# Optimization experiments

Hardware: AMD Instinct MI355X
Metric: run time of the kernel (lower is better)

Reference implementation:

```python
import math
import jax, jax.numpy as jnp
import numpy as np

SR = 48000
FRAME_HOP = 240
F0_MIN = 20.0
F0_MAX = 5000.0
F0_BINS = 64
VEL_DIM = 8
N_HARM = 128
NOISE_FFT = 1024
N_NOISE = NOISE_FFT // 2 + 1
HOP = NOISE_FFT // 4
PAD = NOISE_FFT // 2


def lin_interp(x, size):
    # matches F.interpolate(mode='linear', align_corners=False) along last axis
    T_in = x.shape[-1]
    pos = (jnp.arange(size, dtype=jnp.float32) + 0.5) * (T_in / size) - 0.5
    pos = jnp.clip(pos, 0.0, T_in - 1.0)
    lo = jnp.floor(pos).astype(jnp.int32)
    hi = jnp.minimum(lo + 1, T_in - 1)
    fr = pos - lo.astype(jnp.float32)
    return x[..., lo] * (1.0 - fr) + x[..., hi] * fr


def encode_f0(f0):
    f0s = jnp.clip(f0, F0_MIN, None)
    fn = jnp.clip((jnp.log(f0s) - math.log(F0_MIN)) / (math.log(F0_MAX) - math.log(F0_MIN)), 0.0, 1.0)
    i = jnp.arange(1, F0_BINS // 2 + 1, dtype=jnp.float32)
    ang = math.pi * i * fn[..., None]  # (B,T,bins/2)
    enc = jnp.stack([jnp.sin(ang), jnp.cos(ang)], axis=-1).reshape(f0.shape + (F0_BINS,))
    return enc * (f0 > 0).astype(jnp.float32)[..., None]


def encode_velocity(vel):
    vn = jnp.clip(vel.astype(jnp.float32) / 7.0, 0.0, 1.0)
    i = jnp.arange(1, VEL_DIM // 2 + 1, dtype=jnp.float32)
    ang = math.pi * i * vn[..., None]
    return jnp.stack([jnp.sin(ang), jnp.cos(ang)], axis=-1).reshape(vel.shape + (VEL_DIM,))


def gru(x, W_ih, W_hh, b_ih, b_hh):
    # torch nn.GRU, 1 layer, batch_first; gate order r,z,n
    B, T, _ = x.shape
    H = W_hh.shape[1]
    gi = x @ W_ih.T + b_ih  # (B,T,3H)

    def step(h, g):
        gh = h @ W_hh.T + b_hh
        ir, iz, in_ = jnp.split(g, 3, axis=-1)
        hr, hz, hn = jnp.split(gh, 3, axis=-1)
        r = jax.nn.sigmoid(ir + hr)
        z = jax.nn.sigmoid(iz + hz)
        n = jnp.tanh(in_ + r * hn)
        h = (1.0 - z) * n + z * h
        return h, h

    _, hs = jax.lax.scan(step, jnp.zeros((B, H), x.dtype), jnp.swapaxes(gi, 0, 1))
    return jnp.swapaxes(hs, 0, 1)


def harmonic_synth(harm_amps, f0_hz, n_samples, inh):
    # harm_amps (B,T,N), f0_hz (B,T), inh (B,) -> (B,S)
    B, T, N = harm_amps.shape
    a = lin_interp(jnp.transpose(harm_amps, (0, 2, 1)), n_samples)        # (B,N,S)
    f0_up = lin_interp(f0_hz[:, None, :], n_samples)[:, 0]               # (B,S)
    k = jnp.arange(1, N + 1, dtype=jnp.float32)
    stretch = jnp.sqrt(1.0 + inh[:, None] * k ** 2)                      # (B,N)
    inst_freq = f0_up[:, None, :] * (k[None, :] * stretch)[:, :, None]   # (B,N,S)
    mask = (inst_freq < SR * 0.45).astype(a.dtype)
    f0_mean = f0_up.mean(axis=-1)
    n_active = jnp.maximum((k[None, :] * f0_mean[:, None] < SR * 0.45).sum(axis=1), 1).astype(a.dtype)
    phase = jnp.cumsum(2.0 * jnp.pi * inst_freq / SR, axis=-1)
    sig = (a * mask * jnp.sin(phase)).sum(axis=1)
    return sig / n_active[:, None]


def noise_synth(noise_mags, f0_hz, n_samples, noise):
    # noise_mags (B,T,513), noise (B,S) -> (B,S)
    B, T, N = noise_mags.shape
    window = 0.5 - 0.5 * jnp.cos(2.0 * jnp.pi * jnp.arange(NOISE_FFT, dtype=jnp.float32) / NOISE_FFT)  # hann, periodic
    padded = jnp.pad(noise, ((0, 0), (PAD, PAD)), mode='reflect')
    T_stft = 1 + n_samples // HOP
    idx = jnp.arange(T_stft)[:, None] * HOP + jnp.arange(NOISE_FFT)[None, :]  # (T_stft, n_fft)
    frames = padded[:, idx] * window                                          # (B,T_stft,n_fft)
    spec = jnp.fft.rfft(frames)                                               # (B,T_stft,513)
    mag_up = lin_interp(jnp.transpose(noise_mags, (0, 2, 1)), T_stft)         # (B,513,T_stft)
    f0_mean = jnp.clip(f0_hz, F0_MIN, None).mean(axis=1)                      # (B,)
    freqs = jnp.arange(N_NOISE, dtype=jnp.float32) * (SR / NOISE_FFT)
    src = jnp.clip(freqs[None, :] / f0_mean[:, None] * (N / N_HARM), 0.0, N - 1.0)  # (B,513)
    lo = src.astype(jnp.int32)
    hi = jnp.minimum(lo + 1, N - 1)
    fr = (src - lo.astype(jnp.float32))[:, :, None]
    lo_e = jnp.broadcast_to(lo[:, :, None], (B, N_NOISE, T_stft))
    hi_e = jnp.broadcast_to(hi[:, :, None], (B, N_NOISE, T_stft))
    v_lo = jnp.take_along_axis(mag_up, lo_e, axis=1)
    v_hi = jnp.take_along_axis(mag_up, hi_e, axis=1)
    mag_abs = v_lo + fr * (v_hi - v_lo)                                       # (B,513,T_stft)
    shaped = spec * jnp.transpose(mag_abs, (0, 2, 1))                         # (B,T_stft,513)
    tframes = jnp.fft.irfft(shaped, n=NOISE_FFT) * window                     # (B,T_stft,n_fft)
    Lp = NOISE_FFT + (T_stft - 1) * HOP
    flat = idx.reshape(-1)
    ola = jnp.zeros((B, Lp), jnp.float32).at[:, flat].add(tframes.reshape(B, -1))
    wsq = jnp.zeros((Lp,), jnp.float32).at[flat].add(jnp.tile(window ** 2, T_stft))
    out = ola / jnp.where(wsq > 1e-11, wsq, 1.0)
    return out[:, PAD:PAD + n_samples]


def ddsp_forward(f0_hz, loudness_db, noise_L, noise_R,
                 W_pre1, b_pre1, W_pre2, b_pre2, W_ih, W_hh, b_ih, b_hh,
                 W_post, b_post, W_harm, b_harm, W_amp, b_amp,
                 W_noise, b_noise, W_namp, b_namp, W_B, b_B, velocity):
    B, T = f0_hz.shape
    n_samples = T * FRAME_HOP
    feat = jnp.concatenate([encode_f0(f0_hz),
                            jnp.broadcast_to(encode_velocity(velocity)[:, None, :], (B, T, VEL_DIM))], axis=-1)
    feat = jax.nn.relu(feat @ W_pre1 + b_pre1)
    feat = jax.nn.relu(feat @ W_pre2 + b_pre2)
    feat = gru(feat, W_ih, W_hh, b_ih, b_hh)
    feat = jax.nn.relu(feat @ W_post + b_post)
    # stereo heads stacked on channel axis c in {L,R}
    harm_dist = jax.nn.softmax(jnp.einsum('btd,cdn->cbtn', feat, W_harm) + b_harm[:, None, None, :], axis=-1)
    harm_amp = jax.nn.softplus(jnp.einsum('btd,cd->cbt', feat, W_amp) + b_amp[:, None, None])
    harm_amps = harm_dist * harm_amp[..., None]                               # (2,B,T,128)
    nmag = jax.nn.sigmoid(jnp.einsum('btd,cdn->cbtn', feat, W_noise) + b_noise[:, None, None, :])
    nmag = nmag * jax.nn.softplus(jnp.einsum('btd,cd->cbt', feat, W_namp) + b_namp[:, None, None])[..., None]
    f0_mean = jnp.clip(f0_hz, F0_MIN, None).mean(axis=1)
    midi = 69.0 + 12.0 * jnp.log2(f0_mean / 440.0)
    b_max = 0.0008 * jnp.exp(-(midi - 21.0) / 88.0 * math.log(10.0))
    inh = jax.nn.sigmoid(feat @ W_B + b_B[0]).mean(axis=1) * b_max           # inh_scale = 1.0
    hL = harmonic_synth(harm_amps[0], f0_hz, n_samples, inh)
    hR = harmonic_synth(harm_amps[1], f0_hz, n_samples, inh)
    nL = noise_synth(nmag[0], f0_hz, n_samples, noise_L)
    nR = noise_synth(nmag[1], f0_hz, n_samples, noise_R)
    lo_up = lin_interp((10.0 ** (loudness_db / 20.0))[:, None, :], n_samples)[:, 0]
    return jnp.stack([(hL + nL) * lo_up, (hR + nR) * lo_up], axis=1)         # (B,2,S)


def setup_inputs() -> dict:
    key = jax.random.key(0)
    ks = iter(jax.random.split(key, 40))
    B, T = 2, 400
    S = T * FRAME_HOP
    rnd = lambda shape, s=0.05: jax.random.normal(next(ks), shape, jnp.float32) * s
    d = {}
    d['f0_hz'] = 100.0 + 400.0 * jax.random.uniform(next(ks), (B, T), jnp.float32)
    d['loudness_db'] = -30.0 + 5.0 * jax.random.normal(next(ks), (B, T), jnp.float32)
    d['noise_L'] = jax.random.normal(next(ks), (B, S), jnp.float32)
    d['noise_R'] = jax.random.normal(next(ks), (B, S), jnp.float32)
    d['W_pre1'] = rnd((72, 128)); d['b_pre1'] = rnd((128,))
    d['W_pre2'] = rnd((128, 128)); d['b_pre2'] = rnd((128,))
    d['W_ih'] = rnd((192, 128)); d['W_hh'] = rnd((192, 64))
    d['b_ih'] = rnd((192,)); d['b_hh'] = rnd((192,))
    d['W_post'] = rnd((64, 128)); d['b_post'] = rnd((128,))
    d['W_harm'] = rnd((2, 128, N_HARM)); d['b_harm'] = rnd((2, N_HARM))
    d['W_amp'] = rnd((2, 128)); d['b_amp'] = rnd((2,))
    d['W_noise'] = rnd((2, 128, N_NOISE)); d['b_noise'] = rnd((2, N_NOISE)) - 3.0
    d['W_namp'] = rnd((2, 128)); d['b_namp'] = rnd((2,)) - 3.0
    d['W_B'] = rnd((128,)); d['b_B'] = rnd((1,)) - 5.0
    d['velocity'] = jax.random.randint(next(ks), (B,), 0, 8, dtype=jnp.int32)
    return d


def reference(f0_hz, loudness_db, noise_L, noise_R,
              W_pre1, b_pre1, W_pre2, b_pre2, W_ih, W_hh, b_ih, b_hh,
              W_post, b_post, W_harm, b_harm, W_amp, b_amp,
              W_noise, b_noise, W_namp, b_namp, W_B, b_B, velocity):
    return ddsp_forward(f0_hz, loudness_db, noise_L, noise_R,
                        W_pre1, b_pre1, W_pre2, b_pre2, W_ih, W_hh, b_ih, b_hh,
                        W_post, b_post, W_harm, b_harm, W_amp, b_amp,
                        W_noise, b_noise, W_namp, b_namp, W_B, b_B, velocity)
```

## Files before the change

kernel.cpp:

```cpp
#include <hip/hip_runtime.h>
#include <math.h>

#define Tn   400
#define Bn   2
#define Sn   96000
#define NHh  128
#define NNn  513
#define NFFT 1024
#define HOPs 256
#define PADs 512
#define TS   376
#define LPn  97024
#define CUT  21600.0f
#define DPI  3.14159265358979323846

__device__ __forceinline__ float sigmoidf_(float x){ return 1.0f/(1.0f+expf(-x)); }
__device__ __forceinline__ float softplusf_(float x){ return fmaxf(x,0.0f)+log1pf(expf(-fabsf(x))); }
__device__ __forceinline__ float fsigmoid_(float x){ return __fdividef(1.0f, 1.0f + __expf(-x)); }
__device__ __forceinline__ float ftanh_(float x){
  float e = __expf(fminf(fmaxf(2.0f*x, -30.0f), 30.0f));
  return __fdividef(e - 1.0f, e + 1.0f);
}

__global__ void __launch_bounds__(128) k_frame1z(
    const float* f0, const int* vel,
    const float* Wp1, const float* bp1,
    const float* Wp2, const float* bp2,
    const float* Wih, const float* bih,
    float* gi, float4* olaz, float* fs, double* P) {
  int blk = blockIdx.x;
  int tid = threadIdx.x;
  if (blk >= Bn*Tn) {
    if (blk == Bn*Tn) {
      int b = tid;
      if (b < Bn) {
        const float* f = f0 + b*Tn;
        double sm = 0.0;
        for (int t=0;t<Tn;t++) sm += fmax((double)f[t], 20.0);
        float f0m = (float)(sm / (double)Tn);
        fs[b] = f0m;
        float midi = 69.0f + 12.0f * log2f(f0m/440.0f);
        fs[2+b] = 0.0008f * expf(-(midi-21.0f)*(1.0f/88.0f) * 2.302585093f);
        double* Pb = P + b*Tn;
        double acc = 0.0;
        for (int m=0;m<Tn;m++){ Pb[m] = acc; if (m < Tn-1) acc += (double)f[m] + (double)f[m+1]; }
        double Ctot = 120.0*((double)f[0] + Pb[Tn-1] + (double)f[Tn-1]);
        double fupmean = Ctot / (double)Sn;
        int cnt = 0;
        for (int k=1;k<=NHh;k++) if ((float)k * (float)fupmean < CUT) cnt++;
        if (cnt < 1) cnt = 1;
        fs[4+b] = (float)cnt;
        fs[6+b] = 0.0f;
      }
    } else {
      int base = (blk - (Bn*Tn+1))*512 + tid;
      #pragma unroll
      for (int r=0;r<4;r++) {
        int idx = base + r*128;
        if (idx < 97024) olaz[idx] = make_float4(0.f,0.f,0.f,0.f);
      }
    }
    return;
  }
  int b = blk / Tn, t = blk % Tn;
  __shared__ float x[72];
  __shared__ float y1[128];
  __shared__ float y2[128];
  if (tid < 72) {
    if (tid < 64) {
      float fv = f0[b*Tn+t];
      float fsv = fmaxf(fv, 20.0f);
      float fn = (logf(fsv) - 2.99573227355399f) * (1.0f/5.52146091786225f);
      fn = fminf(fmaxf(fn,0.0f),1.0f);
      int j = (tid>>1) + 1;
      float ang = (float)DPI * (float)j * fn;
      x[tid] = (tid & 1) ? cosf(ang) : sinf(ang);
    } else {
      int i = tid - 64;
      float vn = fminf(fmaxf((float)vel[b]*(1.0f/7.0f),0.0f),1.0f);
      int j = (i>>1)+1;
      float ang = (float)DPI * (float)j * vn;
      x[tid] = (i & 1) ? cosf(ang) : sinf(ang);
    }
  }
  __syncthreads();
  {
    float a = bp1[tid];
    #pragma unroll 8
    for (int i=0;i<72;i++) a += x[i]*Wp1[i*128+tid];
    y1[tid] = fmaxf(a,0.0f);
  }
  __syncthreads();
  {
    float a = bp2[tid];
    #pragma unroll 8
    for (int i=0;i<128;i++) a += y1[i]*Wp2[i*128+tid];
    y2[tid] = fmaxf(a,0.0f);
  }
  __syncthreads();
  float* gout = gi + ((size_t)b*Tn + t)*192;
  for (int g = tid; g < 192; g += 128) {
    float s = bih[g];
    const float* wr = Wih + g*128;
    #pragma unroll 8
    for (int d=0; d<128; d++) s += y2[d]*wr[d];
    gout[g] = s;
  }
}

__global__ void __launch_bounds__(448, 1) k_grufft(
    const float* __restrict__ gi, const float* __restrict__ Whh,
    const float* __restrict__ bhh, float* __restrict__ hsout,
    const float* __restrict__ noiseL, const float* __restrict__ noiseR,
    float2* __restrict__ spec) {
  __shared__ float h[64];
  __shared__ float sp[384];
  __shared__ float re[1024], im[1024];
  __shared__ float twc[512], tws[512];
  __shared__ float wdw[1024];
  int j = threadIdx.x;

  if (blockIdx.x >= 2) {
    if (j >= 256) return;
    int idx = blockIdx.x - 2;
    int sig = idx / TS, t = idx % TS;
    int b = sig >> 1, c = sig & 1;
    const float* noise = (c==0 ? noiseL : noiseR) + (size_t)b*Sn;
    int tid = j;
    for (int q=tid; q<512; q+=256) {
      float ang = (float)(2.0*DPI) * (float)q * (1.0f/1024.0f);
      twc[q] = cosf(ang); tws[q] = sinf(ang);
    }
    for (int i=tid; i<1024; i+=256)
      wdw[i] = 0.5f - 0.5f*cosf((float)(2.0*DPI)*(float)i*(1.0f/1024.0f));
    __syncthreads();
    for (int i=tid;i<1024;i+=256) {
      int q = t*HOPs + i - PADs;
      if (q < 0) q = -q;
      if (q >= Sn) q = 2*Sn - 2 - q;
      float v = noise[q]*wdw[i];
      int br = (int)(__brev((unsigned)i) >> 22);
      re[br] = v; im[br] = 0.0f;
    }
    __syncthreads();
    for (int st=1; st<=10; st++) {
      int half = 1<<(st-1);
      #pragma unroll
      for (int w=0;w<2;w++) {
        int bid = tid + w*256;
        int pos = bid & (half-1);
        int i0 = ((bid >> (st-1)) << st) + pos;
        int i1 = i0 + half;
        int q = pos << (10-st);
        float cr = twc[q], ci = -tws[q];
        float xr = re[i1], xi = im[i1];
        float tr = cr*xr - ci*xi, ti = cr*xi + ci*xr;
        float ar = re[i0], ai = im[i0];
        re[i1] = ar - tr; im[i1] = ai - ti;
        re[i0] = ar + tr; im[i0] = ai + ti;
      }
      __syncthreads();
    }
    float2* so = spec + ((size_t)sig*TS + t)*NNn;
    for (int k=tid;k<=512;k+=256) so[k] = make_float2(re[k], im[k]);
    return;
  }

  int b = blockIdx.x;
  const float* gib = gi + (size_t)b*Tn*192;
  float* hb_ = hsout + (size_t)b*Tn*64;
  int wv = j >> 6, lane = j & 63;
  int p = wv & 1;
  int row = (wv >> 1)*64 + lane;
  float4 w0,w1,w2,w3,w4,w5,w6,w7;
  if (wv < 6) {
    const float4* W4 = (const float4*)(Whh + (size_t)row*64 + p*32);
    w0=W4[0]; w1=W4[1]; w2=W4[2]; w3=W4[3];
    w4=W4[4]; w5=W4[5]; w6=W4[6]; w7=W4[7];
    if (j < 64) h[j] = 0.0f;
  }
  float hu = 0.0f, br=0.f, bz=0.f, bn=0.f;
  float ga[16], gz_[16], gn_[16], hist[16];
  if (wv == 6) {
    br = bhh[lane]; bz = bhh[64+lane]; bn = bhh[128+lane];
    #pragma unroll
    for (int i=0;i<16;i++) {
      ga[i]  = gib[(size_t)i*192 + lane];
      gz_[i] = gib[(size_t)i*192 + 64 + lane];
      gn_[i] = gib[(size_t)i*192 + 128 + lane];
    }
  }
  __syncthreads();

  for (int c=0;c<25;c++) {
    #pragma unroll
    for (int i=0;i<16;i++) {
      if (wv < 6) {
        const float4* h4 = (const float4*)h;
        float4 x0=h4[p*8+0], x1=h4[p*8+1], x2=h4[p*8+2], x3=h4[p*8+3];
        float4 x4=h4[p*8+4], x5=h4[p*8+5], x6=h4[p*8+6], x7=h4[p*8+7];
        float a0,a1,a2,a3;
        a0 = w0.x*x0.x; a1 = w0.y*x0.y; a2 = w0.z*x0.z; a3 = w0.w*x0.w;
        a0 = fmaf(w1.x,x1.x,a0); a1 = fmaf(w1.y,x1.y,a1);
        a2 = fmaf(w1.z,x1.z,a2); a3 = fmaf(w1.w,x1.w,a3);
        a0 = fmaf(w2.x,x2.x,a0); a1 = fmaf(w2.y,x2.y,a1);
        a2 = fmaf(w2.z,x2.z,a2); a3 = fmaf(w2.w,x2.w,a3);
        a0 = fmaf(w3.x,x3.x,a0); a1 = fmaf(w3.y,x3.y,a1);
        a2 = fmaf(w3.z,x3.z,a2); a3 = fmaf(w3.w,x3.w,a3);
        a0 = fmaf(w4.x,x4.x,a0); a1 = fmaf(w4.y,x4.y,a1);
        a2 = fmaf(w4.z,x4.z,a2); a3 = fmaf(w4.w,x4.w,a3);
        a0 = fmaf(w5.x,x5.x,a0); a1 = fmaf(w5.y,x5.y,a1);
        a2 = fmaf(w5.z,x5.z,a2); a3 = fmaf(w5.w,x5.w,a3);
        a0 = fmaf(w6.x,x6.x,a0); a1 = fmaf(w6.y,x6.y,a1);
        a2 = fmaf(w6.z,x6.z,a2); a3 = fmaf(w6.w,x6.w,a3);
        a0 = fmaf(w7.x,x7.x,a0); a1 = fmaf(w7.y,x7.y,a1);
        a2 = fmaf(w7.z,x7.z,a2); a3 = fmaf(w7.w,x7.w,a3);
        sp[p*192 + row] = (a0+a1)+(a2+a3);
      }
      __syncthreads();
      if (wv == 6) {
        float mr = sp[lane]     + sp[192+lane];
        float mz = sp[64+lane]  + sp[256+lane];
        float mn = sp[128+lane] + sp[320+lane];
        float rg = fsigmoid_(ga[i]  + br + mr);
        float zg = fsigmoid_(gz_[i] + bz + mz);
        float ng = ftanh_(gn_[i] + rg*(bn + mn));
        hu = (1.0f - zg)*ng + zg*hu;
        h[lane] = hu;
        hist[i] = hu;
      }
      __syncthreads();
    }
    if (wv == 6) {
      int t0 = c*16;
      #pragma unroll
      for (int i=0;i<16;i++) hb_[(size_t)(t0+i)*64 + lane] = hist[i];
      if (c < 24) {
        int t1 = t0 + 16;
        #pragma unroll
        for (int i=0;i<16;i++) {
          ga[i]  = gib[(size_t)(t1+i)*192 + lane];
          gz_[i] = gib[(size_t)(t1+i)*192 + 64 + lane];
          gn_[i] = gib[(size_t)(t1+i)*192 + 128 + lane];
        }
      }
    }
  }
}

__global__ void __launch_bounds__(256) k_heads(
    const float* hs, const float* Wpost, const float* bpost,
    const float* Wharm, const float* bharm,
    const float* Wamp, const float* bamp,
    const float* Wnoise, const float* bnoise,
    const float* Wnamp, const float* bnamp,
    const float* WB, const float* bB,
    float* harm, float* nmag, float* fs) {
  int bt = blockIdx.x; int b = bt / Tn, t = bt % Tn;
  __shared__ float h64[64];
  __shared__ float fp[128];
  __shared__ float lg[256];
  __shared__ float red[8];
  int tid = threadIdx.x;
  if (tid < 64) h64[tid] = hs[((size_t)b*Tn+t)*64+tid];
  __syncthreads();
  if (tid < 128) {
    float a = bpost[tid];
    #pragma unroll 8
    for (int i=0;i<64;i++) a += h64[i]*Wpost[i*128+tid];
    fp[tid] = fmaxf(a,0.0f);
  }
  __syncthreads();
  {
    int c = tid >> 7, n = tid & 127;
    float a = bharm[c*128+n];
    const float* w = Wharm + (size_t)c*128*128 + n;
    #pragma unroll 8
    for (int d=0;d<128;d++) a += fp[d]*w[d*128];
    lg[tid] = a;
  }
  __syncthreads();
  if (tid < 2) {
    const float* l = lg + tid*128;
    float mx = l[0];
    for (int n=1;n<128;n++) mx = fmaxf(mx,l[n]);
    float sm = 0.f; for (int n=0;n<128;n++) sm += expf(l[n]-mx);
    red[tid] = mx; red[2+tid] = sm;
    float aa = bamp[tid];
    for (int d=0;d<128;d++) aa += fp[d]*Wamp[tid*128+d];
    red[4+tid] = softplusf_(aa);
    float na = bnamp[tid];
    for (int d=0;d<128;d++) na += fp[d]*Wnamp[tid*128+d];
    red[6+tid] = softplusf_(na);
  } else if (tid == 2) {
    float bb = bB[0];
    for (int d=0;d<128;d++) bb += fp[d]*WB[d];
    atomicAdd(&fs[6+b], sigmoidf_(bb));
  }
  __syncthreads();
  {
    int c = tid >> 7, n = tid & 127;
    float v = expf(lg[tid]-red[c]) / red[2+c] * red[4+c];
    harm[(((size_t)c*Bn + b)*Tn + t)*128 + n] = v;
  }
  for (int o = tid; o < 2*NNn; o += 256) {
    int c = (o < NNn) ? 0 : 1; int n = o - c*NNn;
    float a = bnoise[c*NNn+n];
    const float* w = Wnoise + (size_t)c*128*NNn + n;
    #pragma unroll 8
    for (int d=0;d<128;d++) a += fp[d]*w[(size_t)d*NNn];
    nmag[(((size_t)c*Bn + b)*Tn + t)*NNn + n] = sigmoidf_(a) * red[6+c];
  }
}

__global__ void __launch_bounds__(256) k_harmnoise(
    const float* __restrict__ f0, const float* __restrict__ harm,
    const double* __restrict__ P, const float* __restrict__ fs,
    float* __restrict__ sigh,
    const float2* __restrict__ spec, const float* __restrict__ nmag,
    float* __restrict__ ola) {
  __shared__ double rks[128];
  __shared__ float  rkf[128];
  __shared__ float re[1024], im[1024];
  __shared__ float twc[512], tws[512];
  __shared__ float wdw[1024];
  int tid = threadIdx.x;

  if (blockIdx.x < 750) {
    int b = blockIdx.x / 375;
    int s = (blockIdx.x % 375)*256 + tid;
    if (tid < 128) {
      float inhf = fs[6+b]*(1.0f/(float)Tn) * fs[2+b];
      double inh = (double)inhf;
      double kk = (double)(tid+1);
      double r = kk * sqrt(1.0 + inh*kk*kk);
      rks[tid] = r; rkf[tid] = (float)r;
    }
    __syncthreads();
    const float* f = f0 + b*Tn;
    float posf = ((float)s + 0.5f) * (400.0f/96000.0f) - 0.5f;
    posf = fminf(fmaxf(posf, 0.0f), 399.0f);
    int lo = (int)floorf(posf);
    int hi = min(lo+1, 399);
    float fr = posf - (float)lo;
    float f0up = f[lo]*(1.0f-fr) + f[hi]*fr;
    double C;
    if (s < 120) {
      C = (double)(s+1) * (double)f[0];
    } else if (s < 95880) {
      int m = (s-120)/240;
      int q = s - 120 - 240*m;
      double fm = (double)f[m], fm1 = (double)f[m+1];
      double jp = (double)(q+1);
      C = 120.0*((double)f[0] + P[b*Tn+m]) + jp*fm + (fm1-fm)*jp*jp*(1.0/480.0);
    } else {
      C = 120.0*((double)f[0] + P[b*Tn+399]) + (double)(s-95880+1)*(double)f[399];
    }
    double Phi = C * (2.0*DPI/48000.0);
    const float* hLlo = harm + (((size_t)0*Bn + b)*Tn + lo)*128;
    const float* hLhi = harm + (((size_t)0*Bn + b)*Tn + hi)*128;
    const float* hRlo = harm + (((size_t)1*Bn + b)*Tn + lo)*128;
    const float* hRhi = harm + (((size_t)1*Bn + b)*Tn + hi)*128;
    float accL=0.f, accR=0.f;
    for (int k=0;k<128;k++) {
      float finst = f0up * rkf[k];
      if (finst < CUT) {
        double u = rks[k]*Phi * (1.0/(2.0*DPI));
        u -= floor(u);
        float sv = __sinf((float)u * 6.28318530717959f);
        float aL = hLlo[k]*(1.0f-fr) + hLhi[k]*fr;
        float aR = hRlo[k]*(1.0f-fr) + hRhi[k]*fr;
        accL += aL*sv; accR += aR*sv;
      }
    }
    float na = fs[4+b];
    sigh[((size_t)b*2+0)*Sn + s] = accL/na;
    sigh[((size_t)b*2+1)*Sn + s] = accR/na;
    return;
  }

  int idx = blockIdx.x - 750;
  int sig = idx / TS, t = idx % TS;
  int b = sig >> 1, c = sig & 1;
  for (int q=tid; q<512; q+=256) {
    float ang = (float)(2.0*DPI) * (float)q * (1.0f/1024.0f);
    twc[q] = cosf(ang); tws[q] = sinf(ang);
  }
  for (int i=tid; i<1024; i+=256)
    wdw[i] = 0.5f - 0.5f*cosf((float)(2.0*DPI)*(float)i*(1.0f/1024.0f));
  float f0m = fs[b];
  float pp = ((float)t + 0.5f) * (400.0f/376.0f) - 0.5f;
  pp = fminf(fmaxf(pp,0.0f),399.0f);
  int tlo = (int)floorf(pp); int thi = min(tlo+1, 399); float tfr = pp - (float)tlo;
  const float* nm = nmag + (((size_t)c*Bn + b)*Tn)*NNn;
  const float2* so = spec + ((size_t)sig*TS + t)*NNn;
  for (int k=tid;k<=512;k+=256) {
    float src = (float)k * 46.875f / f0m * (513.0f/128.0f);
    src = fminf(fmaxf(src,0.0f),512.0f);
    int flo = (int)src; int fhi = min(flo+1,512); float ffr = src - (float)flo;
    float vlo = nm[(size_t)tlo*NNn+flo]*(1.0f-tfr) + nm[(size_t)thi*NNn+flo]*tfr;
    float vhi = nm[(size_t)tlo*NNn+fhi]*(1.0f-tfr) + nm[(size_t)thi*NNn+fhi]*tfr;
    float mag = vlo + ffr*(vhi-vlo);
    float2 v = so[k];
    re[k] = v.x*mag; im[k] = v.y*mag;
  }
  __syncthreads();
  for (int k=tid+513; k<1024; k+=256) {
    re[k] = re[1024-k]; im[k] = -im[1024-k];
  }
  __syncthreads();
  for (int i=tid;i<1024;i+=256) {
    int jx = (int)(__brev((unsigned)i)>>22);
    if (i < jx) {
      float a=re[i]; re[i]=re[jx]; re[jx]=a;
      float bb=im[i]; im[i]=im[jx]; im[jx]=bb;
    }
  }
  __syncthreads();
  for (int st=1; st<=10; st++) {
    int half = 1<<(st-1);
    #pragma unroll
    for (int w=0;w<2;w++) {
      int bid = tid + w*256;
      int pos = bid & (half-1);
      int i0 = ((bid >> (st-1)) << st) + pos;
      int i1 = i0 + half;
      int q = pos << (10-st);
      float cr = twc[q], ci = tws[q];
      float xr = re[i1], xi = im[i1];
      float tr = cr*xr - ci*xi, ti = cr*xi + ci*xr;
      float ar = re[i0], ai = im[i0];
      re[i1] = ar - tr; im[i1] = ai - ti;
      re[i0] = ar + tr; im[i0] = ai + ti;
    }
    __syncthreads();
  }
  float* olab = ola + (size_t)sig*LPn;
  for (int i=tid;i<1024;i+=256) {
    float y = re[i] * (1.0f/1024.0f) * wdw[i];
    atomicAdd(&olab[t*HOPs + i], y);
  }
}

__global__ void __launch_bounds__(256) k_final(
    const float* loud, const float* sigh, const float* ola, float* out) {
  int b = blockIdx.y;
  int s = blockIdx.x*256 + threadIdx.x;
  float posf = ((float)s + 0.5f)*(400.0f/96000.0f) - 0.5f;
  posf = fminf(fmaxf(posf,0.0f),399.0f);
  int lo=(int)floorf(posf); int hi=min(lo+1,399); float fr=posf-(float)lo;
  const float* ld = loud + b*Tn;
  float lv = exp10f(ld[lo]*0.05f)*(1.0f-fr) + exp10f(ld[hi]*0.05f)*fr;
  int p = PADs + s;
  float wsq;
  if (s >= 511 && s <= 95743) {
    wsq = 1.5f;
  } else {
    int t0 = (p >= 1023) ? ((p - 1023 + 255) >> 8) : 0;
    int t1 = min(TS-1, p >> 8);
    wsq = 0.0f;
    for (int t=t0;t<=t1;t++) {
      int i = p - (t<<8);
      float w = 0.5f - 0.5f*cosf((float)(2.0*DPI)*(float)i*(1.0f/1024.0f));
      wsq += w*w;
    }
  }
  float denom = (wsq > 1e-11f) ? wsq : 1.0f;
  for (int c=0;c<2;c++) {
    float hv = sigh[((size_t)b*2+c)*Sn+s];
    float nv = ola[(size_t)(b*2+c)*LPn + p] / denom;
    out[((size_t)b*2+c)*Sn + s] = (hv + nv)*lv;
  }
}

extern "C" void kernel_launch(void* const* d_in, const int* in_sizes, int n_in,
                              void* d_out, int out_size, void* d_ws, size_t ws_size,
                              hipStream_t stream) {
  const float* f0    = (const float*)d_in[0];
  const float* loud  = (const float*)d_in[1];
  const float* nL    = (const float*)d_in[2];
  const float* nR    = (const float*)d_in[3];
  const float* Wp1   = (const float*)d_in[4];  const float* bp1 = (const float*)d_in[5];
  const float* Wp2   = (const float*)d_in[6];  const float* bp2 = (const float*)d_in[7];
  const float* Wih   = (const float*)d_in[8];  const float* Whh = (const float*)d_in[9];
  const float* bih   = (const float*)d_in[10]; const float* bhh = (const float*)d_in[11];
  const float* Wpost = (const float*)d_in[12]; const float* bpost=(const float*)d_in[13];
  const float* Wharm = (const float*)d_in[14]; const float* bharm=(const float*)d_in[15];
  const float* Wamp  = (const float*)d_in[16]; const float* bamp =(const float*)d_in[17];
  const float* Wnoise= (const float*)d_in[18]; const float* bnoise=(const float*)d_in[19];
  const float* Wnamp = (const float*)d_in[20]; const float* bnamp=(const float*)d_in[21];
  const float* WB    = (const float*)d_in[22]; const float* bB  = (const float*)d_in[23];
  const int*   vel   = (const int*)d_in[24];
  float* out = (float*)d_out;

  char* w = (char*)d_ws;
  double* P    = (double*)w; w += (size_t)Bn*Tn*sizeof(double);
  double* rk   = (double*)w; w += (size_t)Bn*128*sizeof(double);
  float* gi    = (float*)w;  w += (size_t)Bn*Tn*192*sizeof(float);
  float* hsb   = (float*)w;  w += (size_t)Bn*Tn*64*sizeof(float);
  float* harm  = (float*)w;  w += (size_t)2*Bn*Tn*128*sizeof(float);
  float* nmag  = (float*)w;  w += (size_t)2*Bn*Tn*NNn*sizeof(float);
  float* sigh  = (float*)w;  w += (size_t)Bn*2*Sn*sizeof(float);
  float* ola   = (float*)w;  w += (size_t)Bn*2*LPn*sizeof(float);
  float* fscal = (float*)w;  w += 32*sizeof(float);
  float2* spec = (float2*)w; w += (size_t)4*TS*NNn*sizeof(float2);
  (void)rk;

  int nzblk = (97024 + 511) / 512;
  k_frame1z<<<Bn*Tn + 1 + nzblk, 128, 0, stream>>>(
      f0, vel, Wp1,bp1, Wp2,bp2, Wih,bih, gi, (float4*)ola, fscal, P);
  k_grufft<<<2 + 4*TS, 448, 0, stream>>>(gi, Whh, bhh, hsb, nL, nR, spec);
  k_heads<<<Bn*Tn, 256, 0, stream>>>(hsb, Wpost,bpost, Wharm,bharm, Wamp,bamp,
                                     Wnoise,bnoise, Wnamp,bnamp, WB,bB,
                                     harm, nmag, fscal);
  k_harmnoise<<<750 + 4*TS, 256, 0, stream>>>(f0, harm, P, fscal, sigh,
                                              spec, nmag, ola);
  dim3 gf(Sn/256, Bn);
  k_final<<<gf, 256, 0, stream>>>(loud, sigh, ola, out);
}
```

Baseline: 398.9 us.

## Redundantly compute GRU gates in every wave and broadcast hidden state via readlane

Restructures the GRU recurrence block to use 12 waves (768 threads), each holding a 16-wide slice of W_hh. Every wave now computes the gate update redundantly, and the hidden state is broadcast with readlane instead of being staged through shared memory. A double-buffered partial-sum array lets each timestep use one barrier instead of two, which targets the serial per-step sync latency. The cost is a larger block (FFT blocks still return above 256 threads), redundant transcendental math in every wave, and a lot of scalar readlane traffic.

Result: slower. 535.5 us (+34.2%).

```diff
diff --git a/kernel.cpp b/kernel.cpp
--- a/kernel.cpp
+++ b/kernel.cpp
@@ -108,13 +108,14 @@
   }
 }
 
-__global__ void __launch_bounds__(448, 1) k_grufft(
+#define RL(x, l) __int_as_float(__builtin_amdgcn_readlane(__float_as_int(x), (l)))
+
+__global__ void __launch_bounds__(768, 1) k_grufft(
     const float* __restrict__ gi, const float* __restrict__ Whh,
     const float* __restrict__ bhh, float* __restrict__ hsout,
     const float* __restrict__ noiseL, const float* __restrict__ noiseR,
     float2* __restrict__ spec) {
-  __shared__ float h[64];
-  __shared__ float sp[384];
+  __shared__ float sp[2][768];
   __shared__ float re[1024], im[1024];
   __shared__ float twc[512], tws[512];
   __shared__ float wdw[1024];
@@ -170,79 +171,60 @@
   const float* gib = gi + (size_t)b*Tn*192;
   float* hb_ = hsout + (size_t)b*Tn*64;
   int wv = j >> 6, lane = j & 63;
-  int p = wv & 1;
-  int row = (wv >> 1)*64 + lane;
-  float4 w0,w1,w2,w3,w4,w5,w6,w7;
-  if (wv < 6) {
-    const float4* W4 = (const float4*)(Whh + (size_t)row*64 + p*32);
-    w0=W4[0]; w1=W4[1]; w2=W4[2]; w3=W4[3];
-    w4=W4[4]; w5=W4[5]; w6=W4[6]; w7=W4[7];
-    if (j < 64) h[j] = 0.0f;
-  }
-  float hu = 0.0f, br=0.f, bz=0.f, bn=0.f;
+  int p = wv & 3;
+  int row = (wv >> 2)*64 + lane;
+  const float4* W4 = (const float4*)(Whh + (size_t)row*64 + p*16);
+  float4 w0=W4[0], w1=W4[1], w2=W4[2], w3=W4[3];
+  float br = bhh[lane], bz = bhh[64+lane], bn = bhh[128+lane];
+  float hu = 0.0f;
+  int B16 = p*16;
   float ga[16], gz_[16], gn_[16], hist[16];
-  if (wv == 6) {
-    br = bhh[lane]; bz = bhh[64+lane]; bn = bhh[128+lane];
-    #pragma unroll
-    for (int i=0;i<16;i++) {
-      ga[i]  = gib[(size_t)i*192 + lane];
-      gz_[i] = gib[(size_t)i*192 + 64 + lane];
-      gn_[i] = gib[(size_t)i*192 + 128 + lane];
-    }
-  }
-  __syncthreads();
-
+  #pragma unroll
+  for (int i=0;i<16;i++) {
+    ga[i]  = gib[(size_t)i*192 + lane];
+    gz_[i] = gib[(size_t)i*192 + 64 + lane];
+    gn_[i] = gib[(size_t)i*192 + 128 + lane];
+  }
+  int par = 0;
   for (int c=0;c<25;c++) {
     #pragma unroll
     for (int i=0;i<16;i++) {
-      if (wv < 6) {
-        const float4* h4 = (const float4*)h;
-        float4 x0=h4[p*8+0], x1=h4[p*8+1], x2=h4[p*8+2], x3=h4[p*8+3];
-        float4 x4=h4[p*8+4], x5=h4[p*8+5], x6=h4[p*8+6], x7=h4[p*8+7];
-        float a0,a1,a2,a3;
-        a0 = w0.x*x0.x; a1 = w0.y*x0.y; a2 = w0.z*x0.z; a3 = w0.w*x0.w;
-        a0 = fmaf(w1.x,x1.x,a0); a1 = fmaf(w1.y,x1.y,a1);
-        a2 = fmaf(w1.z,x1.z,a2); a3 = fmaf(w1.w,x1.w,a3);
-        a0 = fmaf(w2.x,x2.x,a0); a1 = fmaf(w2.y,x2.y,a1);
-        a2 = fmaf(w2.z,x2.z,a2); a3 = fmaf(w2.w,x2.w,a3);
-        a0 = fmaf(w3.x,x3.x,a0); a1 = fmaf(w3.y,x3.y,a1);
-        a2 = fmaf(w3.z,x3.z,a2); a3 = fmaf(w3.w,x3.w,a3);
-        a0 = fmaf(w4.x,x4.x,a0); a1 = fmaf(w4.y,x4.y,a1);
-        a2 = fmaf(w4.z,x4.z,a2); a3 = fmaf(w4.w,x4.w,a3);
-        a0 = fmaf(w5.x,x5.x,a0); a1 = fmaf(w5.y,x5.y,a1);
-        a2 = fmaf(w5.z,x5.z,a2); a3 = fmaf(w5.w,x5.w,a3);
-        a0 = fmaf(w6.x,x6.x,a0); a1 = fmaf(w6.y,x6.y,a1);
-        a2 = fmaf(w6.z,x6.z,a2); a3 = fmaf(w6.w,x6.w,a3);
-        a0 = fmaf(w7.x,x7.x,a0); a1 = fmaf(w7.y,x7.y,a1);
-        a2 = fmaf(w7.z,x7.z,a2); a3 = fmaf(w7.w,x7.w,a3);
-        sp[p*192 + row] = (a0+a1)+(a2+a3);
-      }
+      float a0,a1,a2,a3;
+      a0 = RL(hu,B16+0)*w0.x;            a1 = RL(hu,B16+1)*w0.y;
+      a2 = RL(hu,B16+2)*w0.z;            a3 = RL(hu,B16+3)*w0.w;
+      a0 = fmaf(RL(hu,B16+4),  w1.x,a0); a1 = fmaf(RL(hu,B16+5),  w1.y,a1);
+      a2 = fmaf(RL(hu,B16+6),  w1.z,a2); a3 = fmaf(RL(hu,B16+7),  w1.w,a3);
+      a0 = fmaf(RL(hu,B16+8),  w2.x,a0); a1 = fmaf(RL(hu,B16+9),  w2.y,a1);
+      a2 = fmaf(RL(hu,B16+10), w2.z,a2); a3 = fmaf(RL(hu,B16+11), w2.w,a3);
+      a0 = fmaf(RL(hu,B16+12), w3.x,a0); a1 = fmaf(RL(hu,B16+13), w3.y,a1);
+      a2 = fmaf(RL(hu,B16+14), w3.z,a2); a3 = fmaf(RL(hu,B16+15), w3.w,a3);
+      sp[par][p*192 + row] = (a0+a1)+(a2+a3);
       __syncthreads();
-      if (wv == 6) {
-        float mr = sp[lane]     + sp[192+lane];
-        float mz = sp[64+lane]  + sp[256+lane];
-        float mn = sp[128+lane] + sp[320+lane];
-        float rg = fsigmoid_(ga[i]  + br + mr);
-        float zg = fsigmoid_(gz_[i] + bz + mz);
-        float ng = ftanh_(gn_[i] + rg*(bn + mn));
-        hu = (1.0f - zg)*ng + zg*hu;
-        h[lane] = hu;
-        hist[i] = hu;
-      }
-      __syncthreads();
-    }
-    if (wv == 6) {
+      float mr = (sp[par][lane]     + sp[par][192+lane])
+               + (sp[par][384+lane] + sp[par][576+lane]);
+      float mz = (sp[par][64+lane]     + sp[par][192+64+lane])
+               + (sp[par][384+64+lane] + sp[par][576+64+lane]);
+      float mn = (sp[par][128+lane]     + sp[par][192+128+lane])
+               + (sp[par][384+128+lane] + sp[par][576+128+lane]);
+      float rg = fsigmoid_(ga[i]  + br + mr);
+      float zg = fsigmoid_(gz_[i] + bz + mz);
+      float ng = ftanh_(gn_[i] + rg*(bn + mn));
+      hu = (1.0f - zg)*ng + zg*hu;
+      hist[i] = hu;
+      par ^= 1;
+    }
+    if (wv == 0) {
       int t0 = c*16;
       #pragma unroll
       for (int i=0;i<16;i++) hb_[(size_t)(t0+i)*64 + lane] = hist[i];
-      if (c < 24) {
-        int t1 = t0 + 16;
-        #pragma unroll
-        for (int i=0;i<16;i++) {
-          ga[i]  = gib[(size_t)(t1+i)*192 + lane];
-          gz_[i] = gib[(size_t)(t1+i)*192 + 64 + lane];
-          gn_[i] = gib[(size_t)(t1+i)*192 + 128 + lane];
-        }
+    }
+    if (c < 24) {
+      int t1 = (c+1)*16;
+      #pragma unroll
+      for (int i=0;i<16;i++) {
+        ga[i]  = gib[(size_t)(t1+i)*192 + lane];
+        gz_[i] = gib[(size_t)(t1+i)*192 + 64 + lane];
+        gn_[i] = gib[(size_t)(t1+i)*192 + 128 + lane];
       }
     }
   }
@@ -509,7 +491,7 @@
   int nzblk = (97024 + 511) / 512;
   k_frame1z<<<Bn*Tn + 1 + nzblk, 128, 0, stream>>>(
       f0, vel, Wp1,bp1, Wp2,bp2, Wih,bih, gi, (float4*)ola, fscal, P);
-  k_grufft<<<2 + 4*TS, 448, 0, stream>>>(gi, Whh, bhh, hsb, nL, nR, spec);
+  k_grufft<<<2 + 4*TS, 768, 0, stream>>>(gi, Whh, bhh, hsb, nL, nR, spec);
   k_heads<<<Bn*Tn, 256, 0, stream>>>(hsb, Wpost,bpost, Wharm,bharm, Wamp,bamp,
                                      Wnoise,bnoise, Wnamp,bnamp, WB,bB,
                                      harm, nmag, fscal);
```
